# Kernel optimization log

Hardware: AMD Instinct MI355X
Metric: run time of the kernel (lower is better)

Reference implementation:

```python
import jax, jax.numpy as jnp
import numpy as np

N_EMBD = 1024
N_EXPERTS = 32
BLOCK_DIM = 32          # n_embd // n_experts, asserted == 32 in source
EXPANSION = 4
HIDDEN = BLOCK_DIM * EXPANSION   # 128
ROUTER_HIDDEN = N_EMBD // 4      # 256
MAX_EXPERTS = 4                  # top-k
B, T = 4, 4096


def quantize_ternary(w):
    # BitNet b1.58 absmean ternary: clip(round(W/gamma), -1, 1) * gamma
    gamma = jnp.abs(w).mean() + 1e-8
    return jnp.clip(jnp.round(w / gamma), -1.0, 1.0) * gamma


def setup_inputs() -> dict:
    key = jax.random.key(0)
    k = jax.random.split(key, 6)
    x = jax.random.normal(k[0], (B, T, N_EMBD), dtype=jnp.float32)
    # router: two Linear layers, init normal(std=0.01)
    w_router1 = 0.01 * jax.random.normal(k[1], (ROUTER_HIDDEN, N_EMBD), dtype=jnp.float32)
    w_router2 = 0.01 * jax.random.normal(k[2], (N_EXPERTS, ROUTER_HIDDEN), dtype=jnp.float32)
    # expert weights: uniform(-1, 1) per source init
    gate_w = jax.random.uniform(k[3], (N_EXPERTS, HIDDEN, BLOCK_DIM), minval=-1.0, maxval=1.0, dtype=jnp.float32)
    up_w = jax.random.uniform(k[4], (N_EXPERTS, HIDDEN, BLOCK_DIM), minval=-1.0, maxval=1.0, dtype=jnp.float32)
    down_w = jax.random.uniform(k[5], (N_EXPERTS, BLOCK_DIM, HIDDEN), minval=-1.0, maxval=1.0, dtype=jnp.float32)
    return {"x": x, "w_router1": w_router1, "w_router2": w_router2,
            "gate_w": gate_w, "up_w": up_w, "down_w": down_w}


def reference(x, w_router1, w_router2, gate_w, up_w, down_w):
    Bb, Tt, C = x.shape
    E = gate_w.shape[0]
    D = gate_w.shape[2]
    # ---- router ----
    logits = jax.nn.silu(jnp.einsum('btc,hc->bth', x, w_router1))
    logits = jnp.einsum('bth,eh->bte', logits, w_router2)      # [B,T,E]
    probs = jax.nn.softmax(logits, axis=-1)
    top_vals, top_idx = jax.lax.top_k(probs, MAX_EXPERTS)
    mask = jax.nn.one_hot(top_idx, E, dtype=probs.dtype).sum(axis=-2)  # [B,T,E]
    masked = probs * mask
    weights = masked / jnp.maximum(masked.sum(axis=-1, keepdims=True), 1e-8)
    # ---- experts (ternary-quantized SwiGLU per 32-d block) ----
    gq = quantize_ternary(gate_w)
    uq = quantize_ternary(up_w)
    dq = quantize_ternary(down_w)
    xb = x.reshape(Bb, Tt, E, D)                               # [B,T,E,32]
    g = jnp.einsum('bted,ehd->bteh', xb, gq)                   # [B,T,E,128]
    u = jnp.einsum('bted,ehd->bteh', xb, uq)
    hid = jax.nn.silu(g) * u
    out = jnp.einsum('bteh,edh->bted', hid, dq)                # [B,T,E,32]
    out = out * weights[..., None]
    return out.reshape(Bb, Tt, C)
```

## Files before the change

### kernel.cpp

```cpp
#include <hip/hip_runtime.h>
#include <math.h>

#define TOKENS 16384
#define C 1024
#define RH 256
#define E 32
#define D 32
#define H 128
#define NEL (E * H * D)
#define BCAP 8192
#define NCHUNK 32

typedef _Float16 f16x4 __attribute__((ext_vector_type(4)));
typedef _Float16 f16x8 __attribute__((ext_vector_type(8)));
typedef float    f32x4 __attribute__((ext_vector_type(4)));

__global__ __launch_bounds__(256) void absum_kernel(
    const float* __restrict__ gate, const float* __restrict__ up,
    const float* __restrict__ down, double* __restrict__ partial) {
    const int which = blockIdx.y;
    const float* src = which == 0 ? gate : (which == 1 ? up : down);
    const float4* src4 = (const float4*)src;
    const int base4 = blockIdx.x * 1024;
    const int tid = threadIdx.x;
    double s = 0.0;
    #pragma unroll
    for (int v = 0; v < 4; ++v) {
        const float4 f = src4[base4 + tid + v * 256];
        s += (double)fabsf(f.x) + (double)fabsf(f.y) +
             (double)fabsf(f.z) + (double)fabsf(f.w);
    }
    __shared__ double red[256];
    red[tid] = s;
    __syncthreads();
    for (int off = 128; off > 0; off >>= 1) {
        if (tid < off) red[tid] += red[tid + off];
        __syncthreads();
    }
    if (tid == 0) partial[which * 32 + blockIdx.x] = red[0];
}

__global__ void gamma_kernel(const double* __restrict__ partial,
                             float* __restrict__ gammaArr, int* __restrict__ counts) {
    const int t = threadIdx.x;
    if (t < 3) {
        double s = 0.0;
        for (int j = 0; j < 32; ++j) s += partial[t * 32 + j];
        gammaArr[t] = (float)(s / (double)NEL) + 1e-8f;
    }
    if (t >= 32) counts[(t - 32) * 16] = 0;
}

__global__ __launch_bounds__(256) void quant_all(
    const float* __restrict__ gate, const float* __restrict__ up,
    const float* __restrict__ down, const float* __restrict__ gammaArr,
    float* __restrict__ gQ, float* __restrict__ uQ, float* __restrict__ dQ) {
    const int idx4 = blockIdx.x * 256 + threadIdx.x;
    const int which = idx4 >> 15;
    const int i4 = idx4 & 32767;
    const float4* s4 = (const float4*)(which == 0 ? gate : (which == 1 ? up : down));
    float4* o4 = (float4*)(which == 0 ? gQ : (which == 1 ? uQ : dQ));
    const float gam = gammaArr[which];
    float4 v = s4[i4];
    v.x = fminf(1.f, fmaxf(-1.f, rintf(v.x / gam))) * gam;
    v.y = fminf(1.f, fmaxf(-1.f, rintf(v.y / gam))) * gam;
    v.z = fminf(1.f, fmaxf(-1.f, rintf(v.z / gam))) * gam;
    v.w = fminf(1.f, fmaxf(-1.f, rintf(v.w / gam))) * gam;
    o4[i4] = v;
}

__global__ __launch_bounds__(256) void gemm1_mfma(
    const float* __restrict__ X, const float* __restrict__ W1,
    float* __restrict__ H1) {
    __shared__ __align__(16) _Float16 smem[12288];
    const int tid  = threadIdx.x;
    const int lane = tid & 63;
    const int wid  = tid >> 6;
    const int row0 = blockIdx.x * 128;
    const int col0 = blockIdx.y * 64;
    const int wm = (wid >> 1) * 64;
    const int wn = (wid & 1) * 32;
    const int lr = lane & 15, q = lane >> 4;

    const float* gsrc[6];
    int wh_[6], wl_[6];
    #pragma unroll
    for (int c = 0; c < 6; ++c) {
        const int id = c * 256 + tid;
        int row, c4, base;
        if (id < 1024) { row = id >> 3; c4 = id & 7; base = 0;
                         gsrc[c] = X  + (long)(row0 + row) * C + c4 * 4; }
        else { const int j = id - 1024; row = j >> 3; c4 = j & 7; base = 8192;
               gsrc[c] = W1 + (long)(col0 + row) * C + c4 * 4; }
        const int s  = (row ^ (row >> 2)) & 3;
        const int kb = c4 >> 1;
        wh_[c] = base + row * 32 + ((kb ^ s) << 3) + (c4 & 1) * 4;
        wl_[c] = wh_[c] + (base ? 2048 : 4096);
    }
    int aA[4], aB[2];
    #pragma unroll
    for (int f = 0; f < 4; ++f) {
        const int row = wm + f * 16 + lr;
        const int s = (row ^ (row >> 2)) & 3;
        aA[f] = row * 32 + ((q ^ s) << 3);
    }
    #pragma unroll
    for (int g = 0; g < 2; ++g) {
        const int n = wn + g * 16 + lr;
        const int s = (n ^ (n >> 2)) & 3;
        aB[g] = 8192 + n * 32 + ((q ^ s) << 3);
    }

    f32x4 acc0[4][2] = {}, acc1[4][2] = {};
    float4 va[6], vb[6];

#define LOADG(V, KT) { _Pragma("unroll") \
    for (int c = 0; c < 6; ++c) V[c] = *(const float4*)(gsrc[c] + (KT)); }

#define STAGE(V) { _Pragma("unroll") \
    for (int c = 0; c < 6; ++c) { \
        const float4 v = V[c]; f16x4 hv, lv; \
        hv[0] = (_Float16)v.x; lv[0] = (_Float16)((v.x - (float)hv[0]) * 2048.f); \
        hv[1] = (_Float16)v.y; lv[1] = (_Float16)((v.y - (float)hv[1]) * 2048.f); \
        hv[2] = (_Float16)v.z; lv[2] = (_Float16)((v.z - (float)hv[2]) * 2048.f); \
        hv[3] = (_Float16)v.w; lv[3] = (_Float16)((v.w - (float)hv[3]) * 2048.f); \
        *(f16x4*)&smem[wh_[c]] = hv; \
        *(f16x4*)&smem[wl_[c]] = lv; } }

#define COMPUTE() { \
    f16x8 bh0 = *(const f16x8*)&smem[aB[0]]; \
    f16x8 bl0 = *(const f16x8*)&smem[aB[0] + 2048]; \
    f16x8 bh1 = *(const f16x8*)&smem[aB[1]]; \
    f16x8 bl1 = *(const f16x8*)&smem[aB[1] + 2048]; \
    _Pragma("unroll") \
    for (int f = 0; f < 4; ++f) { \
        const f16x8 ah = *(const f16x8*)&smem[aA[f]]; \
        const f16x8 al = *(const f16x8*)&smem[aA[f] + 4096]; \
        acc0[f][0] = __builtin_amdgcn_mfma_f32_16x16x32_f16(ah, bh0, acc0[f][0], 0, 0, 0); \
        acc1[f][0] = __builtin_amdgcn_mfma_f32_16x16x32_f16(ah, bl0, acc1[f][0], 0, 0, 0); \
        acc1[f][0] = __builtin_amdgcn_mfma_f32_16x16x32_f16(al, bh0, acc1[f][0], 0, 0, 0); \
        acc0[f][1] = __builtin_amdgcn_mfma_f32_16x16x32_f16(ah, bh1, acc0[f][1], 0, 0, 0); \
        acc1[f][1] = __builtin_amdgcn_mfma_f32_16x16x32_f16(ah, bl1, acc1[f][1], 0, 0, 0); \
        acc1[f][1] = __builtin_amdgcn_mfma_f32_16x16x32_f16(al, bh1, acc1[f][1], 0, 0, 0); \
    } }

    LOADG(va, 0);
    for (int kt = 0; kt < C; kt += 64) {
        STAGE(va);
        LOADG(vb, kt + 32);
        __syncthreads();
        COMPUTE();
        __syncthreads();
        STAGE(vb);
        if (kt + 64 < C) LOADG(va, kt + 64);
        __syncthreads();
        COMPUTE();
        __syncthreads();
    }
    const int crow = (lane >> 4) * 4, ccol = lane & 15;
    #pragma unroll
    for (int f = 0; f < 4; ++f)
        #pragma unroll
        for (int g = 0; g < 2; ++g)
            #pragma unroll
            for (int r = 0; r < 4; ++r) {
                const int m = row0 + wm + f * 16 + crow + r;
                const int n = col0 + wn + g * 16 + ccol;
                const float v = acc0[f][g][r] + acc1[f][g][r] * 4.8828125e-4f;
                H1[(long)m * RH + n] = v / (1.f + __expf(-v));
            }
#undef LOADG
#undef STAGE
#undef COMPUTE
}

__global__ __launch_bounds__(256) void router2_kernel(
    const float* __restrict__ H1, const float* __restrict__ W2,
    float* __restrict__ rw, int* __restrict__ counts, int* __restrict__ bucket) {
    __shared__ __align__(16) float w2t[32 * 292];
    __shared__ int lcnt[32];
    __shared__ int gbase[32];
    const int tid = threadIdx.x;
    for (int i = tid; i < E * RH; i += 256) {
        const int e = i >> 8, hh = i & 255;
        w2t[e * 292 + (hh >> 5) * 36 + (hh & 31)] = W2[i];
    }
    if (tid < 32) lcnt[tid] = 0;
    __syncthreads();
    const int tt = tid >> 3;
    const int g  = tid & 7;
    const int tok = blockIdx.x * 32 + tt;
    float4 xr[8];
    const float4* hp4 = (const float4*)(H1 + (long)tok * RH + g * 32);
    #pragma unroll
    for (int q = 0; q < 8; ++q) xr[q] = hp4[q];
    float l[E];
    #pragma unroll
    for (int e = 0; e < E; ++e) {
        const float4* wp = (const float4*)(w2t + e * 292 + g * 36);
        float acc = 0.f;
        #pragma unroll
        for (int q = 0; q < 8; ++q) {
            const float4 w = wp[q];
            acc = fmaf(xr[q].x, w.x, acc); acc = fmaf(xr[q].y, w.y, acc);
            acc = fmaf(xr[q].z, w.z, acc); acc = fmaf(xr[q].w, w.w, acc);
        }
        float v = acc;
        v += __shfl_xor(v, 1);
        v += __shfl_xor(v, 2);
        v += __shfl_xor(v, 4);
        l[e] = v;
    }
    int ti[4], lr_[4];
    if (g == 0) {
        unsigned chosen = 0u;
        float tv[4];
        #pragma unroll
        for (int s = 0; s < 4; ++s) {
            float best = -1e30f; int bi = 0;
            #pragma unroll
            for (int e = 0; e < E; ++e) {
                const bool ok = (((chosen >> e) & 1u) == 0u) && (l[e] > best);
                best = ok ? l[e] : best;
                bi   = ok ? e    : bi;
            }
            chosen |= 1u << bi;
            tv[s] = best; ti[s] = bi;
        }
        const float m = tv[0];
        const float ev[4] = {__expf(tv[0] - m), __expf(tv[1] - m),
                             __expf(tv[2] - m), __expf(tv[3] - m)};
        const float inv = 1.f / (ev[0] + ev[1] + ev[2] + ev[3]);
        #pragma unroll
        for (int s = 0; s < 4; ++s) {
            rw[tok * 4 + s] = ev[s] * inv;
            lr_[s] = atomicAdd(&lcnt[ti[s]], 1);
        }
    }
    __syncthreads();
    if (tid < 32) {
        const int c = lcnt[tid];
        gbase[tid] = c ? atomicAdd(&counts[tid * 16], c) : 0;
    }
    __syncthreads();
    if (g == 0) {
        #pragma unroll
        for (int s = 0; s < 4; ++s)
            bucket[ti[s] * BCAP + gbase[ti[s]] + lr_[s]] = tok * 4 + s;
    }
}

__global__ void zero_kernel(float4* __restrict__ out, int n4) {
    int i = blockIdx.x * blockDim.x + threadIdx.x;
    const int stride = gridDim.x * blockDim.x;
    for (; i < n4; i += stride) out[i] = make_float4(0.f, 0.f, 0.f, 0.f);
}

__global__ __launch_bounds__(256) void expert_compute(
    const float* __restrict__ X, const float* __restrict__ gQ,
    const float* __restrict__ uQ, const float* __restrict__ dQ,
    const int* __restrict__ counts, const int* __restrict__ bucket,
    const float* __restrict__ rw, float* __restrict__ out) {
    const int e = blockIdx.x;
    const int chunk = blockIdx.y;
    int n = counts[e * 16]; if (n > BCAP) n = BCAP;
    const int per = (n + NCHUNK - 1) / NCHUNK;
    int start = chunk * per; if (start > n) start = n;
    int end = start + per;   if (end > n)   end = n;
    const int tid = threadIdx.x;
    const int h   = tid & 127;
    const int tg2 = tid >> 7;
    const int dpair = tid & 15;
    const int hq    = (tid >> 4) & 3;
    const int tg    = tid >> 6;
    float4 gr[8], ur[8];
    {
        const float4* gp = (const float4*)(gQ + (e << 12) + h * D);
        const float4* up = (const float4*)(uQ + (e << 12) + h * D);
        #pragma unroll
        for (int j = 0; j < 8; ++j) { gr[j] = gp[j]; ur[j] = up[j]; }
    }
    float4 dr0[8], dr1[8];
    {
        const float4* p0 = (const float4*)(dQ + (e << 12) + (dpair * 2) * H + hq * 32);
        const float4* p1 = (const float4*)(dQ + (e << 12) + (dpair * 2 + 1) * H + hq * 32);
        #pragma unroll
        for (int k = 0; k < 8; ++k) { dr0[k] = p0[k]; dr1[k] = p1[k]; }
    }
    __shared__ __align__(16) float xs[16][36];
    __shared__ __align__(16) float hsb[16][132];
    __shared__ int   tok_s[16];
    __shared__ float w_s[16];
    __shared__ int   act_s[16];
    const int niter = (end - start + 15) >> 4;
    for (int it = 0; it < niter; ++it) {
        const int base = start + it * 16;
        if (tid < 16) {
            const int idx = base + tid;
            const int a = idx < end;
            int entry = 0;
            if (a) entry = bucket[e * BCAP + idx];
            tok_s[tid] = a ? (entry >> 2) : 0;
            w_s[tid]   = a ? rw[entry] : 0.f;
            act_s[tid] = a;
        }
        __syncthreads();
        {
            int i = tid;
            #pragma unroll
            for (int r2 = 0; r2 < 2; ++r2, i += 256) {
                const int t = i >> 5, d = i & 31;
                xs[t][d] = X[(long)tok_s[t] * C + e * D + d];
            }
        }
        __syncthreads();
        {
            const int col = (h & ~31) | ((h + 8 * (h >> 5)) & 31);
            #pragma unroll
            for (int j = 0; j < 8; ++j) {
                const int t = tg2 * 8 + j;
                const float4* xv4 = (const float4*)&xs[t][0];
                float ga = 0.f, ua = 0.f;
                #pragma unroll
                for (int q = 0; q < 8; ++q) {
                    const float4 xv = xv4[q];
                    ga = fmaf(xv.x, gr[q].x, ga); ga = fmaf(xv.y, gr[q].y, ga);
                    ga = fmaf(xv.z, gr[q].z, ga); ga = fmaf(xv.w, gr[q].w, ga);
                    ua = fmaf(xv.x, ur[q].x, ua); ua = fmaf(xv.y, ur[q].y, ua);
                    ua = fmaf(xv.z, ur[q].z, ua); ua = fmaf(xv.w, ur[q].w, ua);
                }
                hsb[t][col] = ga / (1.f + __expf(-ga)) * ua;
            }
        }
        __syncthreads();
        #pragma unroll
        for (int j = 0; j < 4; ++j) {
            const int t = tg * 4 + j;
            float p0 = 0.f, p1 = 0.f;
            #pragma unroll
            for (int k = 0; k < 8; ++k) {
                const int cb = hq * 32 + ((4 * k + 8 * hq) & 31);
                const float4 hv = *(const float4*)&hsb[t][cb];
                p0 = fmaf(hv.x, dr0[k].x, p0); p0 = fmaf(hv.y, dr0[k].y, p0);
                p0 = fmaf(hv.z, dr0[k].z, p0); p0 = fmaf(hv.w, dr0[k].w, p0);
                p1 = fmaf(hv.x, dr1[k].x, p1); p1 = fmaf(hv.y, dr1[k].y, p1);
                p1 = fmaf(hv.z, dr1[k].z, p1); p1 = fmaf(hv.w, dr1[k].w, p1);
            }
            p0 += __shfl_xor(p0, 16); p0 += __shfl_xor(p0, 32);
            p1 += __shfl_xor(p1, 16); p1 += __shfl_xor(p1, 32);
            if (hq == 0 && act_s[t]) {
                const float wt = w_s[t];
                float2 o = make_float2(wt * p0, wt * p1);
                *(float2*)&out[(long)tok_s[t] * C + e * D + dpair * 2] = o;
            }
        }
        __syncthreads();
    }
}

extern "C" void kernel_launch(void* const* d_in, const int* in_sizes, int n_in,
                              void* d_out, int out_size, void* d_ws, size_t ws_size,
                              hipStream_t stream) {
    const float* x  = (const float*)d_in[0];
    const float* w1 = (const float*)d_in[1];
    const float* w2 = (const float*)d_in[2];
    const float* gw = (const float*)d_in[3];
    const float* uw = (const float*)d_in[4];
    const float* dw = (const float*)d_in[5];
    float* out = (float*)d_out;

    char* ws = (char*)d_ws;
    float*  gQ    = (float*)(ws);
    float*  uQ    = (float*)(ws + (512 << 10));
    float*  dQ    = (float*)(ws + (1024 << 10));
    float*  H1    = (float*)(ws + (1536 << 10));
    const size_t off = (1536 << 10) + (16 << 20);
    float*  rw    = (float*)(ws + off);
    double* part  = (double*)(ws + off + (256 << 10));
    float*  gamma = (float*) (ws + off + (256 << 10) + 1024);
    int*    counts= (int*)   (ws + off + (256 << 10) + 2048);
    int*    bucket= (int*)   (ws + off + (256 << 10) + 8192);

    absum_kernel<<<dim3(32, 3), 256, 0, stream>>>(gw, uw, dw, part);
    gamma_kernel<<<1, 64, 0, stream>>>(part, gamma, counts);
    quant_all<<<3 * NEL / 1024, 256, 0, stream>>>(gw, uw, dw, gamma, gQ, uQ, dQ);
    gemm1_mfma<<<dim3(TOKENS / 128, RH / 64), 256, 0, stream>>>(x, w1, H1);
    router2_kernel<<<TOKENS / 32, 256, 0, stream>>>(H1, w2, rw, counts, bucket);
    zero_kernel<<<4096, 256, 0, stream>>>((float4*)out, TOKENS * C / 4);
    expert_compute<<<dim3(E, NCHUNK), 256, 0, stream>>>(x, gQ, uQ, dQ, counts, bucket, rw, out);
}
```

Measured before the change: 259.2 us.

## Replace sparse bucketed expert FP32 compute with dense MFMA split-fp16 expert kernel

```diff
diff --git a/kernel.cpp b/kernel.cpp
--- a/kernel.cpp
+++ b/kernel.cpp
@@ -8,8 +8,7 @@
 #define D 32
 #define H 128
 #define NEL (E * H * D)
-#define BCAP 8192
-#define NCHUNK 32
+#define INV2048 4.8828125e-4f
 
 typedef _Float16 f16x4 __attribute__((ext_vector_type(4)));
 typedef _Float16 f16x8 __attribute__((ext_vector_type(8)));
@@ -41,32 +40,42 @@
 }
 
 __global__ void gamma_kernel(const double* __restrict__ partial,
-                             float* __restrict__ gammaArr, int* __restrict__ counts) {
+                             float* __restrict__ gammaArr) {
     const int t = threadIdx.x;
     if (t < 3) {
         double s = 0.0;
         for (int j = 0; j < 32; ++j) s += partial[t * 32 + j];
         gammaArr[t] = (float)(s / (double)NEL) + 1e-8f;
     }
-    if (t >= 32) counts[(t - 32) * 16] = 0;
-}
-
-__global__ __launch_bounds__(256) void quant_all(
+}
+
+__global__ __launch_bounds__(256) void tern_prep(
     const float* __restrict__ gate, const float* __restrict__ up,
     const float* __restrict__ down, const float* __restrict__ gammaArr,
-    float* __restrict__ gQ, float* __restrict__ uQ, float* __restrict__ dQ) {
-    const int idx4 = blockIdx.x * 256 + threadIdx.x;
-    const int which = idx4 >> 15;
-    const int i4 = idx4 & 32767;
-    const float4* s4 = (const float4*)(which == 0 ? gate : (which == 1 ? up : down));
-    float4* o4 = (float4*)(which == 0 ? gQ : (which == 1 ? uQ : dQ));
+    _Float16* __restrict__ gf, _Float16* __restrict__ uf, _Float16* __restrict__ dF) {
+    const int b = blockIdx.x;
+    const int which = b >> 6;
+    const int o = (b & 63) * 2048 + threadIdx.x * 8;
     const float gam = gammaArr[which];
-    float4 v = s4[i4];
-    v.x = fminf(1.f, fmaxf(-1.f, rintf(v.x / gam))) * gam;
-    v.y = fminf(1.f, fmaxf(-1.f, rintf(v.y / gam))) * gam;
-    v.z = fminf(1.f, fmaxf(-1.f, rintf(v.z / gam))) * gam;
-    v.w = fminf(1.f, fmaxf(-1.f, rintf(v.w / gam))) * gam;
-    o4[i4] = v;
+    const float* src;
+    _Float16* dst;
+    if (which == 0)      { src = gate + o; dst = gf + o; }
+    else if (which == 1) { src = up + o;   dst = uf + o; }
+    else {
+        const int e = o >> 12, f = (o >> 9) & 7, l = (o >> 3) & 63;
+        const int d  = (f >> 2) * 16 + (l & 15);
+        const int h0 = (f & 3) * 32 + (l >> 4) * 8;
+        src = down + e * 4096 + d * 128 + h0;
+        dst = dF + o;
+    }
+    const float4 v0 = *(const float4*)src;
+    const float4 v1 = *(const float4*)(src + 4);
+    const float a[8] = {v0.x, v0.y, v0.z, v0.w, v1.x, v1.y, v1.z, v1.w};
+    f16x8 t;
+    #pragma unroll
+    for (int j = 0; j < 8; ++j)
+        t[j] = (_Float16)fminf(1.f, fmaxf(-1.f, rintf(a[j] / gam)));
+    *(f16x8*)dst = t;
 }
 
 __global__ __launch_bounds__(256) void gemm1_mfma(
@@ -166,7 +175,7 @@
             for (int r = 0; r < 4; ++r) {
                 const int m = row0 + wm + f * 16 + crow + r;
                 const int n = col0 + wn + g * 16 + ccol;
-                const float v = acc0[f][g][r] + acc1[f][g][r] * 4.8828125e-4f;
+                const float v = acc0[f][g][r] + acc1[f][g][r] * INV2048;
                 H1[(long)m * RH + n] = v / (1.f + __expf(-v));
             }
 #undef LOADG
@@ -176,20 +185,20 @@
 
 __global__ __launch_bounds__(256) void router2_kernel(
     const float* __restrict__ H1, const float* __restrict__ W2,
-    float* __restrict__ rw, int* __restrict__ counts, int* __restrict__ bucket) {
+    float* __restrict__ rwdT) {
     __shared__ __align__(16) float w2t[32 * 292];
-    __shared__ int lcnt[32];
-    __shared__ int gbase[32];
+    __shared__ int   ids4[32][4];
+    __shared__ float vals4[32][4];
     const int tid = threadIdx.x;
     for (int i = tid; i < E * RH; i += 256) {
         const int e = i >> 8, hh = i & 255;
         w2t[e * 292 + (hh >> 5) * 36 + (hh & 31)] = W2[i];
     }
-    if (tid < 32) lcnt[tid] = 0;
     __syncthreads();
     const int tt = tid >> 3;
     const int g  = tid & 7;
-    const int tok = blockIdx.x * 32 + tt;
+    const int tok0 = blockIdx.x * 32;
+    const int tok = tok0 + tt;
     float4 xr[8];
     const float4* hp4 = (const float4*)(H1 + (long)tok * RH + g * 32);
     #pragma unroll
@@ -211,10 +220,9 @@
         v += __shfl_xor(v, 4);
         l[e] = v;
     }
-    int ti[4], lr_[4];
     if (g == 0) {
         unsigned chosen = 0u;
-        float tv[4];
+        float tv[4]; int ti[4];
         #pragma unroll
         for (int s = 0; s < 4; ++s) {
             float best = -1e30f; int bi = 0;
@@ -233,128 +241,126 @@
         const float inv = 1.f / (ev[0] + ev[1] + ev[2] + ev[3]);
         #pragma unroll
         for (int s = 0; s < 4; ++s) {
-            rw[tok * 4 + s] = ev[s] * inv;
-            lr_[s] = atomicAdd(&lcnt[ti[s]], 1);
+            ids4[tt][s]  = ti[s];
+            vals4[tt][s] = ev[s] * inv;
         }
     }
     __syncthreads();
-    if (tid < 32) {
-        const int c = lcnt[tid];
-        gbase[tid] = c ? atomicAdd(&counts[tid * 16], c) : 0;
+    #pragma unroll
+    for (int i = tid; i < 1024; i += 256) {
+        const int t = i & 31, ee = i >> 5;
+        float v = 0.f;
+        #pragma unroll
+        for (int s = 0; s < 4; ++s) if (ids4[t][s] == ee) v = vals4[t][s];
+        rwdT[(long)ee * TOKENS + tok0 + t] = v;
+    }
+}
+
+__global__ __launch_bounds__(256) void expert_dense(
+    const float* __restrict__ X, const _Float16* __restrict__ gf,
+    const _Float16* __restrict__ uf, const _Float16* __restrict__ dF,
+    const float* __restrict__ gammaArr, const float* __restrict__ rwdT,
+    float* __restrict__ out) {
+    const int e = blockIdx.y;
+    const int tok0 = blockIdx.x * 128;
+    const int tid  = threadIdx.x;
+    const int lane = tid & 63;
+    const int wid  = tid >> 6;
+    const int lr = lane & 15, q = lane >> 4;
+    const float gamg = gammaArr[0], gamu = gammaArr[1], gamd = gammaArr[2];
+
+    __shared__ _Float16 xh[128 * 40];
+    __shared__ _Float16 xl[128 * 40];
+    __shared__ unsigned hidb[4][2048];
+    __shared__ float rws[128];
+
+    f16x8 gfr[8], ufr[8], dfr[8];
+    #pragma unroll
+    for (int t8 = 0; t8 < 8; ++t8) {
+        const int row = e * 128 + t8 * 16 + lr;
+        gfr[t8] = *(const f16x8*)(gf + row * 32 + q * 8);
+        ufr[t8] = *(const f16x8*)(uf + row * 32 + q * 8);
+    }
+    #pragma unroll
+    for (int f = 0; f < 8; ++f)
+        dfr[f] = *(const f16x8*)(dF + ((e * 8 + f) * 64 + lane) * 8);
+
+    {
+        const int row = tid >> 1, part = tid & 1;
+        const float4* s4 = (const float4*)(X + (size_t)(tok0 + row) * C + e * 32 + part * 16);
+        #pragma unroll
+        for (int m = 0; m < 4; ++m) {
+            const float4 v = s4[m];
+            f16x4 hv, lv;
+            hv[0] = (_Float16)v.x; lv[0] = (_Float16)((v.x - (float)hv[0]) * 2048.f);
+            hv[1] = (_Float16)v.y; lv[1] = (_Float16)((v.y - (float)hv[1]) * 2048.f);
+            hv[2] = (_Float16)v.z; lv[2] = (_Float16)((v.z - (float)hv[2]) * 2048.f);
+            hv[3] = (_Float16)v.w; lv[3] = (_Float16)((v.w - (float)hv[3]) * 2048.f);
+            const int db = part * 16 + m * 4;
+            *(f16x4*)&xh[row * 40 + db] = hv;
+            *(f16x4*)&xl[row * 40 + db] = lv;
+        }
+        if (tid < 128) rws[tid] = rwdT[(long)e * TOKENS + tok0 + tid];
     }
     __syncthreads();
-    if (g == 0) {
-        #pragma unroll
-        for (int s = 0; s < 4; ++s)
-            bucket[ti[s] * BCAP + gbase[ti[s]] + lr_[s]] = tok * 4 + s;
-    }
-}
-
-__global__ void zero_kernel(float4* __restrict__ out, int n4) {
-    int i = blockIdx.x * blockDim.x + threadIdx.x;
-    const int stride = gridDim.x * blockDim.x;
-    for (; i < n4; i += stride) out[i] = make_float4(0.f, 0.f, 0.f, 0.f);
-}
-
-__global__ __launch_bounds__(256) void expert_compute(
-    const float* __restrict__ X, const float* __restrict__ gQ,
-    const float* __restrict__ uQ, const float* __restrict__ dQ,
-    const int* __restrict__ counts, const int* __restrict__ bucket,
-    const float* __restrict__ rw, float* __restrict__ out) {
-    const int e = blockIdx.x;
-    const int chunk = blockIdx.y;
-    int n = counts[e * 16]; if (n > BCAP) n = BCAP;
-    const int per = (n + NCHUNK - 1) / NCHUNK;
-    int start = chunk * per; if (start > n) start = n;
-    int end = start + per;   if (end > n)   end = n;
-    const int tid = threadIdx.x;
-    const int h   = tid & 127;
-    const int tg2 = tid >> 7;
-    const int dpair = tid & 15;
-    const int hq    = (tid >> 4) & 3;
-    const int tg    = tid >> 6;
-    float4 gr[8], ur[8];
-    {
-        const float4* gp = (const float4*)(gQ + (e << 12) + h * D);
-        const float4* up = (const float4*)(uQ + (e << 12) + h * D);
-        #pragma unroll
-        for (int j = 0; j < 8; ++j) { gr[j] = gp[j]; ur[j] = up[j]; }
-    }
-    float4 dr0[8], dr1[8];
-    {
-        const float4* p0 = (const float4*)(dQ + (e << 12) + (dpair * 2) * H + hq * 32);
-        const float4* p1 = (const float4*)(dQ + (e << 12) + (dpair * 2 + 1) * H + hq * 32);
-        #pragma unroll
-        for (int k = 0; k < 8; ++k) { dr0[k] = p0[k]; dr1[k] = p1[k]; }
-    }
-    __shared__ __align__(16) float xs[16][36];
-    __shared__ __align__(16) float hsb[16][132];
-    __shared__ int   tok_s[16];
-    __shared__ float w_s[16];
-    __shared__ int   act_s[16];
-    const int niter = (end - start + 15) >> 4;
-    for (int it = 0; it < niter; ++it) {
-        const int base = start + it * 16;
-        if (tid < 16) {
-            const int idx = base + tid;
-            const int a = idx < end;
-            int entry = 0;
-            if (a) entry = bucket[e * BCAP + idx];
-            tok_s[tid] = a ? (entry >> 2) : 0;
-            w_s[tid]   = a ? rw[entry] : 0.f;
-            act_s[tid] = a;
-        }
-        __syncthreads();
-        {
-            int i = tid;
+
+    unsigned* hw = hidb[wid];
+    const int swz = (lr & 7) << 2;
+
+    #pragma unroll
+    for (int it = 0; it < 2; ++it) {
+        const int tokbase = (wid * 2 + it) * 16;
+        const f16x8 bxh = *(const f16x8*)&xh[(tokbase + lr) * 40 + q * 8];
+        const f16x8 bxl = *(const f16x8*)&xl[(tokbase + lr) * 40 + q * 8];
+        #pragma unroll
+        for (int t8 = 0; t8 < 8; ++t8) {
+            const f32x4 z = {0.f, 0.f, 0.f, 0.f};
+            f32x4 gh = __builtin_amdgcn_mfma_f32_16x16x32_f16(gfr[t8], bxh, z, 0, 0, 0);
+            f32x4 gl = __builtin_amdgcn_mfma_f32_16x16x32_f16(gfr[t8], bxl, z, 0, 0, 0);
+            f32x4 uh = __builtin_amdgcn_mfma_f32_16x16x32_f16(ufr[t8], bxh, z, 0, 0, 0);
+            f32x4 ul = __builtin_amdgcn_mfma_f32_16x16x32_f16(ufr[t8], bxl, z, 0, 0, 0);
+            unsigned pk[4];
             #pragma unroll
-            for (int r2 = 0; r2 < 2; ++r2, i += 256) {
-                const int t = i >> 5, d = i & 31;
-                xs[t][d] = X[(long)tok_s[t] * C + e * D + d];
+            for (int r = 0; r < 4; ++r) {
+                const float g = gamg * (gh[r] + gl[r] * INV2048);
+                const float u = gamu * (uh[r] + ul[r] * INV2048);
+                const float hd = g / (1.f + __expf(-g)) * u;
+                union { _Float16 h[2]; unsigned u32; } p;
+                p.h[0] = (_Float16)hd;
+                p.h[1] = (_Float16)((hd - (float)p.h[0]) * 2048.f);
+                pk[r] = p.u32;
             }
-        }
-        __syncthreads();
-        {
-            const int col = (h & ~31) | ((h + 8 * (h >> 5)) & 31);
-            #pragma unroll
-            for (int j = 0; j < 8; ++j) {
-                const int t = tg2 * 8 + j;
-                const float4* xv4 = (const float4*)&xs[t][0];
-                float ga = 0.f, ua = 0.f;
-                #pragma unroll
-                for (int q = 0; q < 8; ++q) {
-                    const float4 xv = xv4[q];
-                    ga = fmaf(xv.x, gr[q].x, ga); ga = fmaf(xv.y, gr[q].y, ga);
-                    ga = fmaf(xv.z, gr[q].z, ga); ga = fmaf(xv.w, gr[q].w, ga);
-                    ua = fmaf(xv.x, ur[q].x, ua); ua = fmaf(xv.y, ur[q].y, ua);
-                    ua = fmaf(xv.z, ur[q].z, ua); ua = fmaf(xv.w, ur[q].w, ua);
-                }
-                hsb[t][col] = ga / (1.f + __expf(-ga)) * ua;
-            }
-        }
-        __syncthreads();
-        #pragma unroll
-        for (int j = 0; j < 4; ++j) {
-            const int t = tg * 4 + j;
-            float p0 = 0.f, p1 = 0.f;
-            #pragma unroll
-            for (int k = 0; k < 8; ++k) {
-                const int cb = hq * 32 + ((4 * k + 8 * hq) & 31);
-                const float4 hv = *(const float4*)&hsb[t][cb];
-                p0 = fmaf(hv.x, dr0[k].x, p0); p0 = fmaf(hv.y, dr0[k].y, p0);
-                p0 = fmaf(hv.z, dr0[k].z, p0); p0 = fmaf(hv.w, dr0[k].w, p0);
-                p1 = fmaf(hv.x, dr1[k].x, p1); p1 = fmaf(hv.y, dr1[k].y, p1);
-                p1 = fmaf(hv.z, dr1[k].z, p1); p1 = fmaf(hv.w, dr1[k].w, p1);
-            }
-            p0 += __shfl_xor(p0, 16); p0 += __shfl_xor(p0, 32);
-            p1 += __shfl_xor(p1, 16); p1 += __shfl_xor(p1, 32);
-            if (hq == 0 && act_s[t]) {
-                const float wt = w_s[t];
-                float2 o = make_float2(wt * p0, wt * p1);
-                *(float2*)&out[(long)tok_s[t] * C + e * D + dpair * 2] = o;
-            }
-        }
-        __syncthreads();
+            const int h0 = t8 * 16 + q * 4;
+            *(uint4*)&hw[lr * 128 + (h0 ^ swz)] = make_uint4(pk[0], pk[1], pk[2], pk[3]);
+        }
+        f32x4 dh0 = {0,0,0,0}, dl0 = {0,0,0,0}, dh1 = {0,0,0,0}, dl1 = {0,0,0,0};
+        #pragma unroll
+        for (int kq = 0; kq < 4; ++kq) {
+            const int h0d = kq * 32 + q * 8;
+            const uint4 wlo = *(const uint4*)&hw[lr * 128 + (h0d ^ swz)];
+            const uint4 whi = *(const uint4*)&hw[lr * 128 + ((h0d + 4) ^ swz)];
+            union { unsigned u[4]; f16x8 v; } ah, al;
+            ah.u[0] = __builtin_amdgcn_perm(wlo.y, wlo.x, 0x05040100u);
+            al.u[0] = __builtin_amdgcn_perm(wlo.y, wlo.x, 0x07060302u);
+            ah.u[1] = __builtin_amdgcn_perm(wlo.w, wlo.z, 0x05040100u);
+            al.u[1] = __builtin_amdgcn_perm(wlo.w, wlo.z, 0x07060302u);
+            ah.u[2] = __builtin_amdgcn_perm(whi.y, whi.x, 0x05040100u);
+            al.u[2] = __builtin_amdgcn_perm(whi.y, whi.x, 0x07060302u);
+            ah.u[3] = __builtin_amdgcn_perm(whi.w, whi.z, 0x05040100u);
+            al.u[3] = __builtin_amdgcn_perm(whi.w, whi.z, 0x07060302u);
+            dh0 = __builtin_amdgcn_mfma_f32_16x16x32_f16(ah.v, dfr[kq],     dh0, 0, 0, 0);
+            dl0 = __builtin_amdgcn_mfma_f32_16x16x32_f16(al.v, dfr[kq],     dl0, 0, 0, 0);
+            dh1 = __builtin_amdgcn_mfma_f32_16x16x32_f16(ah.v, dfr[4 + kq], dh1, 0, 0, 0);
+            dl1 = __builtin_amdgcn_mfma_f32_16x16x32_f16(al.v, dfr[4 + kq], dl1, 0, 0, 0);
+        }
+        #pragma unroll
+        for (int r = 0; r < 4; ++r) {
+            const int trow = tokbase + q * 4 + r;
+            const float w = rws[trow];
+            float* op = out + (size_t)(tok0 + trow) * C + e * 32;
+            op[lr]      = gamd * (dh0[r] + dl0[r] * INV2048) * w;
+            op[16 + lr] = gamd * (dh1[r] + dl1[r] * INV2048) * w;
+        }
     }
 }
 
@@ -370,22 +376,19 @@
     float* out = (float*)d_out;
 
     char* ws = (char*)d_ws;
-    float*  gQ    = (float*)(ws);
-    float*  uQ    = (float*)(ws + (512 << 10));
-    float*  dQ    = (float*)(ws + (1024 << 10));
-    float*  H1    = (float*)(ws + (1536 << 10));
-    const size_t off = (1536 << 10) + (16 << 20);
-    float*  rw    = (float*)(ws + off);
-    double* part  = (double*)(ws + off + (256 << 10));
-    float*  gamma = (float*) (ws + off + (256 << 10) + 1024);
-    int*    counts= (int*)   (ws + off + (256 << 10) + 2048);
-    int*    bucket= (int*)   (ws + off + (256 << 10) + 8192);
+    float*     H1    = (float*)(ws);
+    size_t off = (size_t)16 << 20;
+    _Float16*  gf    = (_Float16*)(ws + off); off += (256 << 10);
+    _Float16*  uf    = (_Float16*)(ws + off); off += (256 << 10);
+    _Float16*  dF    = (_Float16*)(ws + off); off += (256 << 10);
+    float*     rwdT  = (float*)(ws + off);    off += (2 << 20);
+    double*    part  = (double*)(ws + off);   off += 1024;
+    float*     gamma = (float*)(ws + off);
 
     absum_kernel<<<dim3(32, 3), 256, 0, stream>>>(gw, uw, dw, part);
-    gamma_kernel<<<1, 64, 0, stream>>>(part, gamma, counts);
-    quant_all<<<3 * NEL / 1024, 256, 0, stream>>>(gw, uw, dw, gamma, gQ, uQ, dQ);
+    gamma_kernel<<<1, 64, 0, stream>>>(part, gamma);
+    tern_prep<<<192, 256, 0, stream>>>(gw, uw, dw, gamma, gf, uf, dF);
     gemm1_mfma<<<dim3(TOKENS / 128, RH / 64), 256, 0, stream>>>(x, w1, H1);
-    router2_kernel<<<TOKENS / 32, 256, 0, stream>>>(H1, w2, rw, counts, bucket);
-    zero_kernel<<<4096, 256, 0, stream>>>((float4*)out, TOKENS * C / 4);
-    expert_compute<<<dim3(E, NCHUNK), 256, 0, stream>>>(x, gQ, uQ, dQ, counts, bucket, rw, out);
-}
+    router2_kernel<<<TOKENS / 32, 256, 0, stream>>>(H1, w2, rwdT);
+    expert_dense<<<dim3(TOKENS / 128, E), 256, 0, stream>>>(x, gf, uf, dF, gamma, rwdT, out);
+}
```

Result: faster. 238.4 us (-8.1%).
